# Kernel optimization log

Measured on AMD Instinct MI355X. Metric: run time of the kernel, lower is better.

## Reference

```python
import jax, jax.numpy as jnp
import numpy as np

V, E, Hd, B, S = 50000, 256, 256, 128, 128  # vocab, embed, hidden, batch, seq


def setup_inputs() -> dict:
    key = jax.random.key(0)
    ks = jax.random.split(key, 16)
    std = 1.0 / np.sqrt(Hd)

    def u(k, shape, lim):
        return jax.random.uniform(k, shape, jnp.float32, -lim, lim)

    emb_table = jax.random.normal(ks[0], (V, E), jnp.float32)
    emb_table = emb_table.at[0].set(0.0)  # padding_idx=0

    inp = {
        'batch_size': B,
        'input_Q': jax.random.randint(ks[1], (S, B), 0, V),
        'input_C': jax.random.randint(ks[2], (S, B), 0, V),
        'input_C2': jax.random.randint(ks[3], (S, B), 0, V),
        'hidden_Q': jnp.zeros((2, B, Hd), jnp.float32),
        'cell_Q': jnp.zeros((2, B, Hd), jnp.float32),
        'hidden_C': jnp.zeros((2, B, Hd), jnp.float32),
        'cell_C': jnp.zeros((2, B, Hd), jnp.float32),
        'hidden_C2': jnp.zeros((2, B, Hd), jnp.float32),
        'cell_C2': jnp.zeros((2, B, Hd), jnp.float32),
        'emb_table': emb_table,
        'Wih_f': u(ks[4], (4 * Hd, E), std), 'Whh_f': u(ks[5], (4 * Hd, Hd), std),
        'bih_f': u(ks[6], (4 * Hd,), std), 'bhh_f': u(ks[7], (4 * Hd,), std),
        'Wih_b': u(ks[8], (4 * Hd, E), std), 'Whh_b': u(ks[9], (4 * Hd, Hd), std),
        'bih_b': u(ks[10], (4 * Hd,), std), 'bhh_b': u(ks[11], (4 * Hd,), std),
        'S1_W': u(ks[12], (2 * Hd, 2 * Hd), 0.1),  # init_weights: uniform(-0.1, 0.1)
        'S1_b': u(ks[13], (2 * Hd,), 1.0 / np.sqrt(2 * Hd)),
    }
    return inp


def _lstm_dir(xs, h0, c0, Wih, Whh, b):
    # xs: [S,B,E]; single direction LSTM, torch gate order i,f,g,o
    def step(carry, xt):
        h, c = carry
        g = xt @ Wih.T + h @ Whh.T + b  # [B,4H]
        i, f, gg, o = jnp.split(g, 4, axis=-1)
        c = jax.nn.sigmoid(f) * c + jax.nn.sigmoid(i) * jnp.tanh(gg)
        h = jax.nn.sigmoid(o) * jnp.tanh(c)
        return (h, c), h
    _, ys = jax.lax.scan(step, (h0, c0), xs)
    return ys  # [S,B,H]


def _bilstm(x, h0, c0, Wih_f, Whh_f, bih_f, bhh_f, Wih_b, Whh_b, bih_b, bhh_b):
    # x: [B,S,E] -> [B,S,2H]
    xs = jnp.swapaxes(x, 0, 1)
    yf = _lstm_dir(xs, h0[0], c0[0], Wih_f, Whh_f, bih_f + bhh_f)
    yb = _lstm_dir(xs[::-1], h0[1], c0[1], Wih_b, Whh_b, bih_b + bhh_b)[::-1]
    return jnp.swapaxes(jnp.concatenate([yf, yb], axis=-1), 0, 1)


def _attention(Q, C0, S1_W, S1_b):
    # Batched version of the per-sample loop: Q,C0 [B,S,2H]
    C = jnp.tanh(C0 @ S1_W.T + S1_b)                      # tanh(S1(C0))
    Hm = jnp.einsum('bsd,btd->bst', Q, C)                 # Q @ C.T
    AQ = jax.nn.softmax(Hm, axis=-1)                      # softmax over rows (torch dim=1 for 2D)
    AC = jax.nn.softmax(jnp.swapaxes(Hm, 1, 2), axis=-1)  # softmax(H.T)
    MQ = jnp.einsum('bst,btd->bsd', AQ, Q)
    MC = jnp.einsum('bst,btd->bsd', AC, MQ)
    b = Q.shape[0]
    return MQ.reshape(b, -1), MC.reshape(b, -1)


def reference(batch_size, input_Q, input_C, input_C2, hidden_Q, cell_Q,
              hidden_C, cell_C, hidden_C2, cell_C2, emb_table,
              Wih_f, Whh_f, bih_f, bhh_f, Wih_b, Whh_b, bih_b, bhh_b,
              S1_W, S1_b):
    lstm_w = (Wih_f, Whh_f, bih_f, bhh_f, Wih_b, Whh_b, bih_b, bhh_b)
    # forward() transposes [S,B] -> [B,S] before embedding
    q = emb_table[input_Q.T]
    c = emb_table[input_C.T]
    c2 = emb_table[input_C2.T]
    out_q = _bilstm(q, hidden_Q, cell_Q, *lstm_w)
    out_c = _bilstm(c, hidden_C, cell_C, *lstm_w)
    out_c2 = _bilstm(c2, hidden_C2, cell_C2, *lstm_w)
    attn_Q1, attn_C = _attention(out_q, out_c, S1_W, S1_b)
    attn_Q2, attn_C2 = _attention(out_q, out_c2, S1_W, S1_b)
    return (attn_Q1, attn_C, attn_Q2, attn_C2)
```

## Files before the change

kernel.cpp:

```cpp
#include <hip/hip_runtime.h>
#include <math.h>

namespace {

constexpr int S = 128;
constexpr int B = 128;
constexpr int E = 256;
constexpr int H = 256;

typedef unsigned short u16;
typedef __attribute__((ext_vector_type(8))) short short8v;
typedef __attribute__((ext_vector_type(4))) float f32x4;

__device__ __forceinline__ float sigmoidf(float x) { return 1.0f / (1.0f + expf(-x)); }
__device__ __forceinline__ u16 bf16rnd(float x) {
  unsigned u = __float_as_uint(x);
  return (u16)((u + 0x7FFFu + ((u >> 16) & 1u)) >> 16);
}
__device__ __forceinline__ float bf2f(u16 v) { return __uint_as_float(((unsigned)v) << 16); }
__device__ __forceinline__ void split2(float x, u16& h, u16& l) {
  h = bf16rnd(x);
  l = bf16rnd(x - bf2f(h));
}
__device__ __forceinline__ int gcol_of(int c) {
  return ((c >> 4) & 3) * 256 + ((c & 15) + ((c >> 6) << 4));
}


__global__ void split_pair(const float* __restrict__ src, u16* __restrict__ h,
                           u16* __restrict__ l, long n) {
  long i = (long)blockIdx.x * 256 + threadIdx.x;
  if (i < n) split2(src[i], h[i], l[i]);
}

__global__ void split_w_int(const float* __restrict__ W, u16* __restrict__ h,
                            u16* __restrict__ l) {
  int i = blockIdx.x * 256 + threadIdx.x;
  int c = i >> 8, k = i & 255;
  split2(W[gcol_of(c) * 256 + k], h[i], l[i]);
}

__global__ void make_bint(const float* __restrict__ bih, const float* __restrict__ bhh,
                          float* __restrict__ bint) {
  int c = blockIdx.x * 256 + threadIdx.x;
  int g = gcol_of(c);
  bint[c] = bih[g] + bhh[g];
}

__global__ void init_hc(const float* hQ, const float* cQ, const float* hC, const float* cC,
                        const float* hC2, const float* cC2,
                        u16* hH, u16* hL, float* cst) {
  int i = blockIdx.x * 256 + threadIdx.x;
  if (i >= 6 * B * H) return;
  int z = i / (B * H);
  int rem = i - z * (B * H);
  int input = z >> 1, dir = z & 1;
  const float* hs = input == 0 ? hQ : (input == 1 ? hC : hC2);
  const float* cs = input == 0 ? cQ : (input == 1 ? cC : cC2);
  split2(hs[dir * B * H + rem], hH[i], hL[i]);
  cst[i] = cs[dir * B * H + rem];
}

__global__ void zero_gen(int* gen) {
  if (threadIdx.x < 6) gen[threadIdx.x * 256] = 0;
}


#define MFMA_PROLOG                                        \
  const int tid = threadIdx.x;                             \
  const int wave = tid >> 6, lane = tid & 63;              \
  const int wr = wave >> 1, wc = wave & 1;                 \
  const int lrow = lane & 15, lk = lane >> 4;              \
  f32x4 acc[4][4];

#define MFMA_ZERO_ACC                                      \
  _Pragma("unroll") for (int a_ = 0; a_ < 4; ++a_)         \
  _Pragma("unroll") for (int b_ = 0; b_ < 4; ++b_)         \
      acc[a_][b_] = (f32x4){0.f, 0.f, 0.f, 0.f};

#define MFMA_INNER                                                             \
  __syncthreads();                                                             \
  short8v ah[4], al[4];                                                        \
  _Pragma("unroll") for (int mt = 0; mt < 4; ++mt) {                           \
    int r_ = wr * 64 + mt * 16 + lrow;                                         \
    ah[mt] = *(const short8v*)&Ah[r_ * 40 + lk * 8];                           \
    al[mt] = *(const short8v*)&Al[r_ * 40 + lk * 8];                           \
  }                                                                            \
  _Pragma("unroll") for (int nt = 0; nt < 4; ++nt) {                           \
    int c_ = wc * 64 + nt * 16 + lrow;                                         \
    short8v bh = *(const short8v*)&Bh[c_ * 40 + lk * 8];                       \
    short8v bl = *(const short8v*)&Bl[c_ * 40 + lk * 8];                       \
    _Pragma("unroll") for (int mt = 0; mt < 4; ++mt) {                         \
      acc[mt][nt] = __builtin_amdgcn_mfma_f32_16x16x32_bf16(ah[mt], bh, acc[mt][nt], 0, 0, 0); \
      acc[mt][nt] = __builtin_amdgcn_mfma_f32_16x16x32_bf16(ah[mt], bl, acc[mt][nt], 0, 0, 0); \
      acc[mt][nt] = __builtin_amdgcn_mfma_f32_16x16x32_bf16(al[mt], bh, acc[mt][nt], 0, 0, 0); \
    }                                                                          \
  }

__global__ __launch_bounds__(256) void lstm_fused(
    const int* __restrict__ idxQ, const int* __restrict__ idxC, const int* __restrict__ idxC2,
    const u16* __restrict__ embH, const u16* __restrict__ embL,
    const u16* __restrict__ wihHf, const u16* __restrict__ wihLf,
    const u16* __restrict__ wihHb, const u16* __restrict__ wihLb,
    const u16* __restrict__ whhHf, const u16* __restrict__ whhLf,
    const u16* __restrict__ whhHb, const u16* __restrict__ whhLb,
    const float* __restrict__ bintf, const float* __restrict__ bintb,
    u16* __restrict__ hH, u16* __restrict__ hL, const float* __restrict__ cst0,
    u16* __restrict__ out3h, u16* __restrict__ out3l,
    int* __restrict__ gen)
{
  const int bx = blockIdx.x;
  const int z = bx & 7;
  if (z >= 6) return;
  const int nb = bx >> 3;
  const int input = z >> 1, dir = z & 1;
  const int n0c = nb * 64;
  const int tid = threadIdx.x;
  const int wave = tid >> 6, lane = tid & 63;
  const int lrow = lane & 15, lk = lane >> 4;
  const int wr = wave;
  const int* idx = input == 0 ? idxQ : (input == 1 ? idxC : idxC2);
  const u16* wiHp = dir ? wihHb : wihHf;
  const u16* wiLp = dir ? wihLb : wihLf;
  const u16* whHp = dir ? whhHb : whhHf;
  const u16* whLp = dir ? whhLb : whhLf;
  const float* bint = dir ? bintb : bintf;

  __shared__ __align__(16) short WiH[64 * 264], WiL[64 * 264];
  __shared__ __align__(16) short WhH[64 * 264], WhL[64 * 264];
  __shared__ int tok[128];

#pragma unroll
  for (int i = 0; i < 8; ++i) {
    int e = i * 256 + tid;
    int c = e >> 5, kc = e & 31;
    long src = (long)(n0c + c) * 256 + kc * 8;
    *(short8v*)&WiH[c * 264 + kc * 8] = *(const short8v*)(wiHp + src);
    *(short8v*)&WiL[c * 264 + kc * 8] = *(const short8v*)(wiLp + src);
    *(short8v*)&WhH[c * 264 + kc * 8] = *(const short8v*)(whHp + src);
    *(short8v*)&WhL[c * 264 + kc * 8] = *(const short8v*)(whLp + src);
  }

  const int u = nb * 16 + lrow;
  float bintv[4];
#pragma unroll
  for (int nt = 0; nt < 4; ++nt) bintv[nt] = bint[n0c + nt * 16 + lrow];

  const long HS = (long)6 * B * H;
  const long zb = (long)z * B * H;
  float creg[2][4];
#pragma unroll
  for (int mt = 0; mt < 2; ++mt)
#pragma unroll
    for (int rg = 0; rg < 4; ++rg)
      creg[mt][rg] = cst0[zb + (long)(wr * 32 + mt * 16 + lk * 4 + rg) * H + u];

  int* genz = gen + z * 256;
  u16* o3h = out3h + (long)input * B * S * 512;
  u16* o3l = out3l + (long)input * B * S * 512;

  __syncthreads();

  for (int t = 0; t < S; ++t) {
    const int t_eff = dir ? (S - 1 - t) : t;
    const int par = t & 1;

    if (tid < 128) tok[tid] = idx[t_eff * B + tid];
    __syncthreads();
    const int tv0 = tok[wr * 32 + lrow];
    const int tv1 = tok[wr * 32 + 16 + lrow];

    f32x4 acc[2][4];
#pragma unroll
    for (int mt = 0; mt < 2; ++mt)
#pragma unroll
      for (int nt = 0; nt < 4; ++nt)
        acc[mt][nt] = (f32x4){bintv[nt], bintv[nt], bintv[nt], bintv[nt]};

#pragma unroll
    for (int kb = 0; kb < 8; ++kb) {
      short8v ah[2], al[2];
      {
        long e0 = (long)tv0 * 256 + kb * 32 + lk * 8;
        long e1 = (long)tv1 * 256 + kb * 32 + lk * 8;
        ah[0] = *(const short8v*)(embH + e0);
        al[0] = *(const short8v*)(embL + e0);
        ah[1] = *(const short8v*)(embH + e1);
        al[1] = *(const short8v*)(embL + e1);
      }
#pragma unroll
      for (int nt = 0; nt < 4; ++nt) {
        int c = nt * 16 + lrow;
        short8v bh = *(const short8v*)&WiH[c * 264 + kb * 32 + lk * 8];
        short8v bl = *(const short8v*)&WiL[c * 264 + kb * 32 + lk * 8];
#pragma unroll
        for (int mt = 0; mt < 2; ++mt) {
          acc[mt][nt] = __builtin_amdgcn_mfma_f32_16x16x32_bf16(ah[mt], bh, acc[mt][nt], 0, 0, 0);
          acc[mt][nt] = __builtin_amdgcn_mfma_f32_16x16x32_bf16(ah[mt], bl, acc[mt][nt], 0, 0, 0);
          acc[mt][nt] = __builtin_amdgcn_mfma_f32_16x16x32_bf16(al[mt], bh, acc[mt][nt], 0, 0, 0);
        }
      }
    }

    if (t > 0) {
      if (tid == 0) {
        const int target = 16 * t;
        while (__hip_atomic_load(genz, __ATOMIC_ACQUIRE, __HIP_MEMORY_SCOPE_AGENT) < target) {
          __builtin_amdgcn_s_sleep(2);
        }
      }
      __syncthreads();
    }

    const u16* hrH = hH + (long)par * HS + zb;
    const u16* hrL = hL + (long)par * HS + zb;
#pragma unroll
    for (int kb = 0; kb < 8; ++kb) {
      short8v ah[2], al[2];
#pragma unroll
      for (int mt = 0; mt < 2; ++mt) {
        long ho = (long)(wr * 32 + mt * 16 + lrow) * 256 + kb * 32 + lk * 8;
        ah[mt] = *(const short8v*)(hrH + ho);
        al[mt] = *(const short8v*)(hrL + ho);
      }
#pragma unroll
      for (int nt = 0; nt < 4; ++nt) {
        int c = nt * 16 + lrow;
        short8v bh = *(const short8v*)&WhH[c * 264 + kb * 32 + lk * 8];
        short8v bl = *(const short8v*)&WhL[c * 264 + kb * 32 + lk * 8];
#pragma unroll
        for (int mt = 0; mt < 2; ++mt) {
          acc[mt][nt] = __builtin_amdgcn_mfma_f32_16x16x32_bf16(ah[mt], bh, acc[mt][nt], 0, 0, 0);
          acc[mt][nt] = __builtin_amdgcn_mfma_f32_16x16x32_bf16(ah[mt], bl, acc[mt][nt], 0, 0, 0);
          acc[mt][nt] = __builtin_amdgcn_mfma_f32_16x16x32_bf16(al[mt], bh, acc[mt][nt], 0, 0, 0);
        }
      }
    }

    u16* hwH = hH + (long)(par ^ 1) * HS + zb;
    u16* hwL = hL + (long)(par ^ 1) * HS + zb;
#pragma unroll
    for (int mt = 0; mt < 2; ++mt)
#pragma unroll
      for (int rg = 0; rg < 4; ++rg) {
        int row = wr * 32 + mt * 16 + lk * 4 + rg;
        float ig = sigmoidf(acc[mt][0][rg]);
        float fg = sigmoidf(acc[mt][1][rg]);
        float gg = tanhf(acc[mt][2][rg]);
        float og = sigmoidf(acc[mt][3][rg]);
        float cn = fg * creg[mt][rg] + ig * gg;
        creg[mt][rg] = cn;
        float hn = og * tanhf(cn);
        u16 hh, hl;
        split2(hn, hh, hl);
        long ci = (long)row * H + u;
        hwH[ci] = hh;
        hwL[ci] = hl;
        long oi = ((long)row * S + t_eff) * 512 + dir * 256 + u;
        o3h[oi] = hh;
        o3l[oi] = hl;
      }

    asm volatile("s_waitcnt vmcnt(0)" ::: "memory");
    __syncthreads();
    if (tid == 0) {
      __hip_atomic_fetch_add(genz, 1, __ATOMIC_RELEASE, __HIP_MEMORY_SCOPE_AGENT);
    }
  }
}

__global__ __launch_bounds__(256) void ct_mfma(
    const u16* __restrict__ aH, const u16* __restrict__ aL,
    const u16* __restrict__ s1H, const u16* __restrict__ s1L,
    const float* __restrict__ s1b,
    u16* __restrict__ ctH, u16* __restrict__ ctL)
{
  const int n0 = blockIdx.x * 128, m0 = blockIdx.y * 128;
  __shared__ __align__(16) short Ah[128 * 40], Al[128 * 40], Bh[128 * 40], Bl[128 * 40];
  MFMA_PROLOG
  MFMA_ZERO_ACC

  for (int kb = 0; kb < 512; kb += 32) {
    __syncthreads();
#pragma unroll
    for (int i = 0; i < 2; ++i) {
      int e = i * 256 + tid;
      int r = e >> 2, kg = e & 3;
      long abase = (long)(m0 + r) * 512 + kb + kg * 8;
      *(short8v*)&Ah[r * 40 + kg * 8] = *(const short8v*)(aH + abase);
      *(short8v*)&Al[r * 40 + kg * 8] = *(const short8v*)(aL + abase);
      long bbase = (long)(n0 + r) * 512 + kb + kg * 8;
      *(short8v*)&Bh[r * 40 + kg * 8] = *(const short8v*)(s1H + bbase);
      *(short8v*)&Bl[r * 40 + kg * 8] = *(const short8v*)(s1L + bbase);
    }
    MFMA_INNER
  }

#pragma unroll
  for (int mt = 0; mt < 4; ++mt)
#pragma unroll
    for (int nt = 0; nt < 4; ++nt) {
      int c = n0 + wc * 64 + nt * 16 + lrow;
      float bv = s1b[c];
#pragma unroll
      for (int rg = 0; rg < 4; ++rg) {
        long m = m0 + wr * 64 + mt * 16 + lk * 4 + rg;
        u16 hh, ll;
        split2(tanhf(acc[mt][nt][rg] + bv), hh, ll);
        ctH[m * 512 + c] = hh;
        ctL[m * 512 + c] = ll;
      }
    }
}

__global__ __launch_bounds__(256) void hm_mfma(
    const u16* __restrict__ qH, const u16* __restrict__ qL,
    const u16* __restrict__ ctH, const u16* __restrict__ ctL,
    float* __restrict__ Hm)
{
  const int bb = blockIdx.x;
  const u16* aH = qH + (long)bb * S * 512;
  const u16* aL = qL + (long)bb * S * 512;
  const u16* bH = ctH + (long)bb * S * 512;
  const u16* bL = ctL + (long)bb * S * 512;
  __shared__ __align__(16) short Ah[128 * 40], Al[128 * 40], Bh[128 * 40], Bl[128 * 40];
  MFMA_PROLOG
  MFMA_ZERO_ACC

  for (int kb = 0; kb < 512; kb += 32) {
    __syncthreads();
#pragma unroll
    for (int i = 0; i < 2; ++i) {
      int e = i * 256 + tid;
      int r = e >> 2, kg = e & 3;
      long base = (long)r * 512 + kb + kg * 8;
      *(short8v*)&Ah[r * 40 + kg * 8] = *(const short8v*)(aH + base);
      *(short8v*)&Al[r * 40 + kg * 8] = *(const short8v*)(aL + base);
      *(short8v*)&Bh[r * 40 + kg * 8] = *(const short8v*)(bH + base);
      *(short8v*)&Bl[r * 40 + kg * 8] = *(const short8v*)(bL + base);
    }
    MFMA_INNER
  }

  float* out = Hm + (long)bb * S * S;
#pragma unroll
  for (int mt = 0; mt < 4; ++mt)
#pragma unroll
    for (int nt = 0; nt < 4; ++nt) {
      int c = wc * 64 + nt * 16 + lrow;
#pragma unroll
      for (int rg = 0; rg < 4; ++rg) {
        int m = wr * 64 + mt * 16 + lk * 4 + rg;
        out[(long)m * S + c] = acc[mt][nt][rg];
      }
    }
}

__global__ void transpose_qt(const u16* __restrict__ o3h, const u16* __restrict__ o3l,
                             u16* __restrict__ qth, u16* __restrict__ qtl) {
  const int b = blockIdx.z;
  const int c0 = blockIdx.x * 64, t0 = blockIdx.y * 64;
  __shared__ u16 tile[64][72];
  const int tid = threadIdx.x;
  for (int pl = 0; pl < 2; ++pl) {
    const u16* src = (pl ? o3l : o3h) + (long)b * S * 512;
    u16* dst = (pl ? qtl : qth) + (long)b * 512 * 128;
    __syncthreads();
#pragma unroll
    for (int i = 0; i < 2; ++i) {
      int e = i * 256 + tid;
      int r = e >> 3, sg = e & 7;
      *(short8v*)&tile[r][sg * 8] = *(const short8v*)(src + (long)(t0 + r) * 512 + c0 + sg * 8);
    }
    __syncthreads();
#pragma unroll
    for (int i = 0; i < 2; ++i) {
      int e = i * 256 + tid;
      int c = e >> 3, sg = e & 7;
      short8v v;
#pragma unroll
      for (int j = 0; j < 8; ++j) v[j] = tile[sg * 8 + j][c];
      *(short8v*)(dst + (long)(c0 + c) * 128 + t0 + sg * 8) = v;
    }
  }
}

template <bool WRITE_T>
__global__ __launch_bounds__(256) void pq_mfma(
    const u16* __restrict__ pH, const u16* __restrict__ pL,
    const u16* __restrict__ btH, const u16* __restrict__ btL,
    float* __restrict__ Cout, u16* __restrict__ tH, u16* __restrict__ tL)
{
  const int bb = blockIdx.z, n0 = blockIdx.x * 128;
  const u16* aHp = pH + (long)bb * 128 * 128;
  const u16* aLp = pL + (long)bb * 128 * 128;
  const u16* bHp = btH + ((long)bb * 512 + n0) * 128;
  const u16* bLp = btL + ((long)bb * 512 + n0) * 128;
  __shared__ __align__(16) short Ah[128 * 40], Al[128 * 40], Bh[128 * 40], Bl[128 * 40];
  MFMA_PROLOG
  MFMA_ZERO_ACC

  for (int kb = 0; kb < 128; kb += 32) {
    __syncthreads();
#pragma unroll
    for (int i = 0; i < 2; ++i) {
      int e = i * 256 + tid;
      int r = e >> 2, kg = e & 3;
      long base = (long)r * 128 + kb + kg * 8;
      *(short8v*)&Ah[r * 40 + kg * 8] = *(const short8v*)(aHp + base);
      *(short8v*)&Al[r * 40 + kg * 8] = *(const short8v*)(aLp + base);
      *(short8v*)&Bh[r * 40 + kg * 8] = *(const short8v*)(bHp + base);
      *(short8v*)&Bl[r * 40 + kg * 8] = *(const short8v*)(bLp + base);
    }
    MFMA_INNER
  }

  float* co = Cout + (long)bb * 128 * 512;
#pragma unroll
  for (int mt = 0; mt < 4; ++mt)
#pragma unroll
    for (int nt = 0; nt < 4; ++nt) {
      int c = n0 + wc * 64 + nt * 16 + lrow;
#pragma unroll
      for (int rg = 0; rg < 4; ++rg) {
        int m = wr * 64 + mt * 16 + lk * 4 + rg;
        float v = acc[mt][nt][rg];
        co[(long)m * 512 + c] = v;
        if (WRITE_T) {
          u16 hh, ll;
          split2(v, hh, ll);
          tH[((long)bb * 512 + c) * 128 + m] = hh;
          tL[((long)bb * 512 + c) * 128 + m] = ll;
        }
      }
    }
}

__global__ void softmax_row_bf(const float* __restrict__ Hm, u16* __restrict__ ph,
                               u16* __restrict__ pl) {
  const int row = blockIdx.x;
  const float* p = Hm + (long)row * S;
  const int l = threadIdx.x;
  float v0 = p[l], v1 = p[l + 64];
  float m = fmaxf(v0, v1);
#pragma unroll
  for (int o = 32; o > 0; o >>= 1) m = fmaxf(m, __shfl_xor(m, o));
  float e0 = expf(v0 - m), e1 = expf(v1 - m);
  float s = e0 + e1;
#pragma unroll
  for (int o = 32; o > 0; o >>= 1) s += __shfl_xor(s, o);
  float inv = 1.0f / s;
  u16 hh, ll;
  split2(e0 * inv, hh, ll);
  ph[(long)row * S + l] = hh; pl[(long)row * S + l] = ll;
  split2(e1 * inv, hh, ll);
  ph[(long)row * S + l + 64] = hh; pl[(long)row * S + l + 64] = ll;
}

__global__ void softmax_colT_bf(const float* __restrict__ Hm, u16* __restrict__ ph,
                                u16* __restrict__ pl) {
  const int b = blockIdx.x >> 7;
  const int col = blockIdx.x & 127;
  const float* p = Hm + (long)b * S * S + col;
  const int l = threadIdx.x;
  float v0 = p[(long)l * S], v1 = p[(long)(l + 64) * S];
  float m = fmaxf(v0, v1);
#pragma unroll
  for (int o = 32; o > 0; o >>= 1) m = fmaxf(m, __shfl_xor(m, o));
  float e0 = expf(v0 - m), e1 = expf(v1 - m);
  float s = e0 + e1;
#pragma unroll
  for (int o = 32; o > 0; o >>= 1) s += __shfl_xor(s, o);
  float inv = 1.0f / s;
  long q = ((long)b * S + col) * S;
  u16 hh, ll;
  split2(e0 * inv, hh, ll);
  ph[q + l] = hh; pl[q + l] = ll;
  split2(e1 * inv, hh, ll);
  ph[q + l + 64] = hh; pl[q + l + 64] = ll;
}

__global__ void softmax_row(const float* __restrict__ Hm, float* __restrict__ A) {
  const int row = blockIdx.x;
  const float* p = Hm + (long)row * S;
  const int l = threadIdx.x;
  float v0 = p[l], v1 = p[l + 64];
  float m = fmaxf(v0, v1);
#pragma unroll
  for (int o = 32; o > 0; o >>= 1) m = fmaxf(m, __shfl_xor(m, o));
  float e0 = expf(v0 - m), e1 = expf(v1 - m);
  float s = e0 + e1;
#pragma unroll
  for (int o = 32; o > 0; o >>= 1) s += __shfl_xor(s, o);
  float inv = 1.0f / s;
  float* q = A + (long)row * S;
  q[l] = e0 * inv; q[l + 64] = e1 * inv;
}

__global__ void softmax_colT(const float* __restrict__ Hm, float* __restrict__ A) {
  const int b = blockIdx.x >> 7;
  const int col = blockIdx.x & 127;
  const float* p = Hm + (long)b * S * S + col;
  const int l = threadIdx.x;
  float v0 = p[(long)l * S], v1 = p[(long)(l + 64) * S];
  float m = fmaxf(v0, v1);
#pragma unroll
  for (int o = 32; o > 0; o >>= 1) m = fmaxf(m, __shfl_xor(m, o));
  float e0 = expf(v0 - m), e1 = expf(v1 - m);
  float s = e0 + e1;
#pragma unroll
  for (int o = 32; o > 0; o >>= 1) s += __shfl_xor(s, o);
  float inv = 1.0f / s;
  float* q = A + ((long)b * S + col) * S;
  q[l] = e0 * inv; q[l + 64] = e1 * inv;
}


__global__ void init_state(const float* hQ, const float* cQ,
                           const float* hC, const float* cC,
                           const float* hC2, const float* cC2,
                           float* h0, float* c0) {
  int i = blockIdx.x * 256 + threadIdx.x;
  if (i >= 6 * B * H) return;
  int z = i / (B * H);
  int rem = i - z * (B * H);
  int input = z >> 1, dir = z & 1;
  const float* hs = input == 0 ? hQ : (input == 1 ? hC : hC2);
  const float* cs = input == 0 ? cQ : (input == 1 ? cC : cC2);
  h0[i] = hs[dir * B * H + rem];
  c0[i] = cs[dir * B * H + rem];
}

__global__ __launch_bounds__(256) void lstm_step(
    const int* __restrict__ idxQ, const int* __restrict__ idxC, const int* __restrict__ idxC2,
    const float* __restrict__ emb,
    const float* __restrict__ Wih_f, const float* __restrict__ Whh_f,
    const float* __restrict__ bih_f, const float* __restrict__ bhh_f,
    const float* __restrict__ Wih_b, const float* __restrict__ Whh_b,
    const float* __restrict__ bih_b, const float* __restrict__ bhh_b,
    const float* __restrict__ hread, float* __restrict__ hwrite,
    float* __restrict__ cstate, float* __restrict__ out3, int t)
{
  const int z = blockIdx.z;
  const int input = z >> 1, dir = z & 1;
  const int u0 = blockIdx.x * 16;
  const int b0 = blockIdx.y * 64;
  const int t_eff = dir ? (S - 1 - t) : t;
  const int* idx = input == 0 ? idxQ : (input == 1 ? idxC : idxC2);
  const float* Wih = dir ? Wih_b : Wih_f;
  const float* Whh = dir ? Whh_b : Whh_f;
  const float* bih = dir ? bih_b : bih_f;
  const float* bhh = dir ? bhh_b : bhh_f;

  __shared__ float Alds[64][68];
  __shared__ float Wl[64][68];
  __shared__ int tok[64];

  const int tid = threadIdx.x;
  if (tid < 64) tok[tid] = idx[t_eff * B + b0 + tid];

  const int uu = tid & 15;
  const int rg = tid >> 4;
  const int u = u0 + uu;

  float acc[4][4];
#pragma unroll
  for (int ri = 0; ri < 4; ++ri)
#pragma unroll
    for (int g = 0; g < 4; ++g)
      acc[ri][g] = bih[g * 256 + u] + bhh[g * 256 + u];

  for (int kc = 0; kc < 8; ++kc) {
    __syncthreads();
    if (kc < 4) {
      const int kb = kc * 64;
#pragma unroll
      for (int i = 0; i < 16; ++i) {
        int e = i * 256 + tid;
        int kk = e & 63, r = e >> 6;
        Alds[r][kk] = emb[(long)tok[r] * E + kb + kk];
      }
    } else {
      const int kb = (kc - 4) * 64;
      const float* hs = hread + ((long)z * B + b0) * H + kb;
#pragma unroll
      for (int i = 0; i < 16; ++i) {
        int e = i * 256 + tid;
        int kk = e & 63, r = e >> 6;
        Alds[r][kk] = hs[r * H + kk];
      }
    }
    {
      const float* Wsrc = (kc < 4) ? Wih : Whh;
      const int kb = (kc & 3) * 64;
#pragma unroll
      for (int i = 0; i < 16; ++i) {
        int e = i * 256 + tid;
        int kk = e & 63, c = e >> 6;
        int gcol = (c >> 4) * 256 + u0 + (c & 15);
        Wl[c][kk] = Wsrc[(long)gcol * H + kb + kk];
      }
    }
    __syncthreads();
#pragma unroll
    for (int k4 = 0; k4 < 64; k4 += 4) {
      float4 a[4], w[4];
#pragma unroll
      for (int ri = 0; ri < 4; ++ri) a[ri] = *(const float4*)&Alds[rg * 4 + ri][k4];
#pragma unroll
      for (int g = 0; g < 4; ++g) w[g] = *(const float4*)&Wl[g * 16 + uu][k4];
#pragma unroll
      for (int ri = 0; ri < 4; ++ri)
#pragma unroll
        for (int g = 0; g < 4; ++g)
          acc[ri][g] += a[ri].x * w[g].x + a[ri].y * w[g].y
                      + a[ri].z * w[g].z + a[ri].w * w[g].w;
    }
  }

  float* cs = cstate + (long)z * B * H;
  float* hw = hwrite + (long)z * B * H;
  float* op = out3 + (long)input * B * S * 2 * H;
#pragma unroll
  for (int ri = 0; ri < 4; ++ri) {
    int b = b0 + rg * 4 + ri;
    float ig = sigmoidf(acc[ri][0]);
    float fg = sigmoidf(acc[ri][1]);
    float gg = tanhf(acc[ri][2]);
    float og = sigmoidf(acc[ri][3]);
    float cn = fg * cs[b * H + u] + ig * gg;
    float hn = og * tanhf(cn);
    cs[b * H + u] = cn;
    hw[b * H + u] = hn;
    op[((long)b * S + t_eff) * (2 * H) + dir * H + u] = hn;
  }
}

template <bool TANH>
__global__ __launch_bounds__(256) void gemm_nt(
    const float* __restrict__ A, const float* __restrict__ B_,
    const float* __restrict__ bias, float* __restrict__ C,
    int lda, int ldb, int ldc, int K, long sA, long sB, long sC)
{
  A += blockIdx.z * sA; B_ += blockIdx.z * sB; C += blockIdx.z * sC;
  const int n0 = blockIdx.x * 64, m0 = blockIdx.y * 64;
  __shared__ float Alds[64][68], Blds[64][68];
  const int tid = threadIdx.x, uu = tid & 15, rg = tid >> 4;
  float acc[4][4] = {};
  for (int kb = 0; kb < K; kb += 64) {
    __syncthreads();
#pragma unroll
    for (int i = 0; i < 16; ++i) {
      int e = i * 256 + tid;
      int kk = e & 63, r = e >> 6;
      Alds[r][kk] = A[(long)(m0 + r) * lda + kb + kk];
      Blds[r][kk] = B_[(long)(n0 + r) * ldb + kb + kk];
    }
    __syncthreads();
#pragma unroll
    for (int k4 = 0; k4 < 64; k4 += 4) {
      float4 a[4], w[4];
#pragma unroll
      for (int ri = 0; ri < 4; ++ri) a[ri] = *(const float4*)&Alds[rg * 4 + ri][k4];
#pragma unroll
      for (int ci = 0; ci < 4; ++ci) w[ci] = *(const float4*)&Blds[ci * 16 + uu][k4];
#pragma unroll
      for (int ri = 0; ri < 4; ++ri)
#pragma unroll
        for (int ci = 0; ci < 4; ++ci)
          acc[ri][ci] += a[ri].x * w[ci].x + a[ri].y * w[ci].y
                       + a[ri].z * w[ci].z + a[ri].w * w[ci].w;
    }
  }
#pragma unroll
  for (int ri = 0; ri < 4; ++ri) {
    int m = m0 + rg * 4 + ri;
#pragma unroll
    for (int ci = 0; ci < 4; ++ci) {
      int n = n0 + ci * 16 + uu;
      float v = acc[ri][ci];
      if (bias) v += bias[n];
      if (TANH) v = tanhf(v);
      C[(long)m * ldc + n] = v;
    }
  }
}

__global__ __launch_bounds__(256) void gemm_nn(
    const float* __restrict__ A, const float* __restrict__ B_,
    float* __restrict__ C,
    int lda, int ldb, int ldc, int K, long sA, long sB, long sC)
{
  A += blockIdx.z * sA; B_ += blockIdx.z * sB; C += blockIdx.z * sC;
  const int n0 = blockIdx.x * 64, m0 = blockIdx.y * 64;
  __shared__ float Alds[64][68];
  __shared__ float Blds[64][68];
  const int tid = threadIdx.x, uu = tid & 15, rg = tid >> 4;
  float acc[4][4] = {};
  for (int kb = 0; kb < K; kb += 64) {
    __syncthreads();
#pragma unroll
    for (int i = 0; i < 16; ++i) {
      int e = i * 256 + tid;
      int kk = e & 63, r = e >> 6;
      Alds[r][kk] = A[(long)(m0 + r) * lda + kb + kk];
      Blds[r][kk] = B_[(long)(kb + r) * ldb + n0 + kk];
    }
    __syncthreads();
#pragma unroll
    for (int kk = 0; kk < 64; ++kk) {
      float4 w = *(const float4*)&Blds[kk][uu * 4];
      float a0 = Alds[rg * 4 + 0][kk], a1 = Alds[rg * 4 + 1][kk];
      float a2 = Alds[rg * 4 + 2][kk], a3 = Alds[rg * 4 + 3][kk];
      acc[0][0] += a0 * w.x; acc[0][1] += a0 * w.y; acc[0][2] += a0 * w.z; acc[0][3] += a0 * w.w;
      acc[1][0] += a1 * w.x; acc[1][1] += a1 * w.y; acc[1][2] += a1 * w.z; acc[1][3] += a1 * w.w;
      acc[2][0] += a2 * w.x; acc[2][1] += a2 * w.y; acc[2][2] += a2 * w.z; acc[2][3] += a2 * w.w;
      acc[3][0] += a3 * w.x; acc[3][1] += a3 * w.y; acc[3][2] += a3 * w.z; acc[3][3] += a3 * w.w;
    }
  }
#pragma unroll
  for (int ri = 0; ri < 4; ++ri) {
    int m = m0 + rg * 4 + ri;
    float4 v = make_float4(acc[ri][0], acc[ri][1], acc[ri][2], acc[ri][3]);
    *(float4*)&C[(long)m * ldc + n0 + uu * 4] = v;
  }
}

}

extern "C" void kernel_launch(void* const* d_in, const int* in_sizes, int n_in,
                              void* d_out, int out_size, void* d_ws, size_t ws_size,
                              hipStream_t stream) {
  const int* idxQ    = (const int*)d_in[1];
  const int* idxC    = (const int*)d_in[2];
  const int* idxC2   = (const int*)d_in[3];
  const float* hQ    = (const float*)d_in[4];
  const float* cQ    = (const float*)d_in[5];
  const float* hC    = (const float*)d_in[6];
  const float* cC    = (const float*)d_in[7];
  const float* hC2   = (const float*)d_in[8];
  const float* cC2   = (const float*)d_in[9];
  const float* emb   = (const float*)d_in[10];
  const float* Wih_f = (const float*)d_in[11];
  const float* Whh_f = (const float*)d_in[12];
  const float* bih_f = (const float*)d_in[13];
  const float* bhh_f = (const float*)d_in[14];
  const float* Wih_b = (const float*)d_in[15];
  const float* Whh_b = (const float*)d_in[16];
  const float* bih_b = (const float*)d_in[17];
  const float* bhh_b = (const float*)d_in[18];
  const float* S1W   = (const float*)d_in[19];
  const float* S1b   = (const float*)d_in[20];
  float* out = (float*)d_out;

  const long V = 50000;
  const long OUT1 = (long)B * S * 2 * H;

  size_t off = 0;
  auto alloc = [&](size_t bytes) { size_t o = off; off += (bytes + 255) & ~(size_t)255; return o; };
  const size_t o_o3h  = alloc((size_t)3 * B * S * 512 * 2);
  const size_t o_o3l  = alloc((size_t)3 * B * S * 512 * 2);
  const size_t o_embH = alloc((size_t)V * E * 2);
  const size_t o_embL = alloc((size_t)V * E * 2);
  const size_t o_wihHf = alloc(1024 * 256 * 2), o_wihLf = alloc(1024 * 256 * 2);
  const size_t o_wihHb = alloc(1024 * 256 * 2), o_wihLb = alloc(1024 * 256 * 2);
  const size_t o_whhHf = alloc(1024 * 256 * 2), o_whhLf = alloc(1024 * 256 * 2);
  const size_t o_whhHb = alloc(1024 * 256 * 2), o_whhLb = alloc(1024 * 256 * 2);
  const size_t o_s1H  = alloc(512 * 512 * 2), o_s1L = alloc(512 * 512 * 2);
  const size_t o_bintf = alloc(1024 * 4), o_bintb = alloc(1024 * 4);
  const size_t o_hH   = alloc((size_t)2 * 6 * B * H * 2);
  const size_t o_hL   = alloc((size_t)2 * 6 * B * H * 2);
  const size_t o_cst  = alloc((size_t)6 * B * H * 4);
  const size_t o_gen  = alloc(6 * 256 * 4);
  const size_t o_ctH  = alloc((size_t)B * S * 512 * 2);
  const size_t o_ctL  = alloc((size_t)B * S * 512 * 2);
  const size_t o_Hm   = alloc((size_t)B * S * S * 4);
  const size_t o_Ph   = alloc((size_t)B * S * S * 2);
  const size_t o_Pl   = alloc((size_t)B * S * S * 2);
  const size_t o_QtH  = alloc((size_t)B * 512 * 128 * 2);
  const size_t o_QtL  = alloc((size_t)B * 512 * 128 * 2);
  const size_t o_MQtH = alloc((size_t)B * 512 * 128 * 2);
  const size_t o_MQtL = alloc((size_t)B * 512 * 128 * 2);
  const size_t need_fast = off;

  if (ws_size >= need_fast) {
    char* base = (char*)d_ws;
    u16* o3h = (u16*)(base + o_o3h);
    u16* o3l = (u16*)(base + o_o3l);
    u16* embH = (u16*)(base + o_embH);
    u16* embL = (u16*)(base + o_embL);
    u16* wihHf = (u16*)(base + o_wihHf); u16* wihLf = (u16*)(base + o_wihLf);
    u16* wihHb = (u16*)(base + o_wihHb); u16* wihLb = (u16*)(base + o_wihLb);
    u16* whhHf = (u16*)(base + o_whhHf); u16* whhLf = (u16*)(base + o_whhLf);
    u16* whhHb = (u16*)(base + o_whhHb); u16* whhLb = (u16*)(base + o_whhLb);
    u16* s1H = (u16*)(base + o_s1H); u16* s1L = (u16*)(base + o_s1L);
    float* bintf = (float*)(base + o_bintf);
    float* bintb = (float*)(base + o_bintb);
    u16* hH = (u16*)(base + o_hH);
    u16* hL = (u16*)(base + o_hL);
    float* cst = (float*)(base + o_cst);
    int* gen = (int*)(base + o_gen);
    u16* ctH = (u16*)(base + o_ctH);
    u16* ctL = (u16*)(base + o_ctL);
    float* Hm = (float*)(base + o_Hm);
    u16* Ph = (u16*)(base + o_Ph);
    u16* Pl = (u16*)(base + o_Pl);
    u16* QtH = (u16*)(base + o_QtH);
    u16* QtL = (u16*)(base + o_QtL);
    u16* MQtH = (u16*)(base + o_MQtH);
    u16* MQtL = (u16*)(base + o_MQtL);

    split_pair<<<(int)((V * E + 255) / 256), 256, 0, stream>>>(emb, embH, embL, V * E);
    split_w_int<<<1024, 256, 0, stream>>>(Wih_f, wihHf, wihLf);
    split_w_int<<<1024, 256, 0, stream>>>(Wih_b, wihHb, wihLb);
    split_w_int<<<1024, 256, 0, stream>>>(Whh_f, whhHf, whhLf);
    split_w_int<<<1024, 256, 0, stream>>>(Whh_b, whhHb, whhLb);
    split_pair<<<1024, 256, 0, stream>>>(S1W, s1H, s1L, 512 * 512);
    make_bint<<<4, 256, 0, stream>>>(bih_f, bhh_f, bintf);
    make_bint<<<4, 256, 0, stream>>>(bih_b, bhh_b, bintb);
    init_hc<<<(6 * B * H + 255) / 256, 256, 0, stream>>>(hQ, cQ, hC, cC, hC2, cC2, hH, hL, cst);
    zero_gen<<<1, 64, 0, stream>>>(gen);

    {
      const int* a0 = idxQ; const int* a1 = idxC; const int* a2 = idxC2;
      const u16* a3 = embH; const u16* a4 = embL;
      const u16* a5 = wihHf; const u16* a6 = wihLf;
      const u16* a7 = wihHb; const u16* a8 = wihLb;
      const u16* a9 = whhHf; const u16* a10 = whhLf;
      const u16* a11 = whhHb; const u16* a12 = whhLb;
      const float* a13 = bintf; const float* a14 = bintb;
      u16* a15 = hH; u16* a16 = hL; const float* a17 = cst;
      u16* a18 = o3h; u16* a19 = o3l; int* a20 = gen;
      void* kargs[] = {(void*)&a0, (void*)&a1, (void*)&a2, (void*)&a3, (void*)&a4,
                       (void*)&a5, (void*)&a6, (void*)&a7, (void*)&a8, (void*)&a9,
                       (void*)&a10, (void*)&a11, (void*)&a12, (void*)&a13, (void*)&a14,
                       (void*)&a15, (void*)&a16, (void*)&a17, (void*)&a18, (void*)&a19,
                       (void*)&a20};
      hipLaunchCooperativeKernel((const void*)lstm_fused, dim3(128), dim3(256),
                                 kargs, 0, stream);
    }

    transpose_qt<<<dim3(8, 2, 128), 256, 0, stream>>>(o3h, o3l, QtH, QtL);
    for (int p = 0; p < 2; ++p) {
      const u16* aH = o3h + (size_t)(1 + p) * B * S * 512;
      const u16* aL = o3l + (size_t)(1 + p) * B * S * 512;
      ct_mfma<<<dim3(4, 128), 256, 0, stream>>>(aH, aL, s1H, s1L, S1b, ctH, ctL);
      hm_mfma<<<128, 256, 0, stream>>>(o3h, o3l, ctH, ctL, Hm);
      softmax_row_bf<<<B * S, 64, 0, stream>>>(Hm, Ph, Pl);
      float* MQ = out + (long)(2 * p) * OUT1;
      pq_mfma<true><<<dim3(4, 1, 128), 256, 0, stream>>>(
          Ph, Pl, QtH, QtL, MQ, MQtH, MQtL);
      softmax_colT_bf<<<B * S, 64, 0, stream>>>(Hm, Ph, Pl);
      float* MC = out + (long)(2 * p + 1) * OUT1;
      pq_mfma<false><<<dim3(4, 1, 128), 256, 0, stream>>>(
          Ph, Pl, MQtH, MQtL, MC, nullptr, nullptr);
    }
    return;
  }

  const long ST = (long)6 * B * H;
  float* ws    = (float*)d_ws;
  float* out3  = ws;
  float* hbuf0 = out3 + 3 * OUT1;
  float* hbuf1 = hbuf0 + ST;
  float* cbuf  = hbuf1 + ST;
  float* Ct    = cbuf + ST;
  float* Hm    = Ct + OUT1;
  float* Ab    = Hm + (long)B * S * S;

  init_state<<<(6 * B * H + 255) / 256, 256, 0, stream>>>(hQ, cQ, hC, cC, hC2, cC2, hbuf0, cbuf);

  for (int t = 0; t < S; ++t) {
    float* hr = (t & 1) ? hbuf1 : hbuf0;
    float* hw = (t & 1) ? hbuf0 : hbuf1;
    lstm_step<<<dim3(16, 2, 6), 256, 0, stream>>>(
        idxQ, idxC, idxC2, emb,
        Wih_f, Whh_f, bih_f, bhh_f, Wih_b, Whh_b, bih_b, bhh_b,
        hr, hw, cbuf, out3, t);
  }

  for (int p = 0; p < 2; ++p) {
    const float* Q  = out3;
    const float* C0 = out3 + (long)(1 + p) * OUT1;
    gemm_nt<true><<<dim3(8, 256, 1), 256, 0, stream>>>(
        C0, S1W, S1b, Ct, 512, 512, 512, 512, 0, 0, 0);
    gemm_nt<false><<<dim3(2, 2, B), 256, 0, stream>>>(
        Q, Ct, nullptr, Hm, 512, 512, 128, 512,
        (long)S * 512, (long)S * 512, (long)S * S);
    softmax_row<<<B * S, 64, 0, stream>>>(Hm, Ab);
    float* MQ = out + (long)(2 * p) * OUT1;
    gemm_nn<<<dim3(8, 2, B), 256, 0, stream>>>(
        Ab, Q, MQ, 128, 512, 512, 128,
        (long)S * S, (long)S * 512, (long)S * 512);
    softmax_colT<<<B * S, 64, 0, stream>>>(Hm, Ab);
    float* MC = out + (long)(2 * p + 1) * OUT1;
    gemm_nn<<<dim3(8, 2, B), 256, 0, stream>>>(
        Ab, MQ, MC, 128, 512, 512, 128,
        (long)S * S, (long)S * 512, (long)S * 512);
  }
}
```

Measured before the change: 2.240 ms.

## Pack hidden state hi/lo into 32-bit words with relaxed atomics for cross-block sync

Packs the bf16 hi/lo split of the recurrent hidden state into one 32-bit word so each exchange is a single relaxed atomic store or load instead of two arrays. The spin-wait and generation counter drop from acquire/release to relaxed ordering with a shorter sleep. The per-step token staging through shared memory and its barrier go away, and the output stores move after the generation increment so they no longer delay the signal. Relaxed atomics instead of acquire/release could risk memory-visibility bugs, and the packed loads need extra unpacking ALU work.

```diff
diff --git a/kernel.cpp b/kernel.cpp
--- a/kernel.cpp
+++ b/kernel.cpp
@@ -9,8 +9,10 @@
 constexpr int H = 256;
 
 typedef unsigned short u16;
+typedef unsigned long long u64;
 typedef __attribute__((ext_vector_type(8))) short short8v;
 typedef __attribute__((ext_vector_type(4))) float f32x4;
+typedef __attribute__((ext_vector_type(4))) unsigned uint4v;
 
 __device__ __forceinline__ float sigmoidf(float x) { return 1.0f / (1.0f + expf(-x)); }
 __device__ __forceinline__ u16 bf16rnd(float x) {
@@ -49,7 +51,7 @@
 
 __global__ void init_hc(const float* hQ, const float* cQ, const float* hC, const float* cC,
                         const float* hC2, const float* cC2,
-                        u16* hH, u16* hL, float* cst) {
+                        unsigned* hP, float* cst) {
   int i = blockIdx.x * 256 + threadIdx.x;
   if (i >= 6 * B * H) return;
   int z = i / (B * H);
@@ -57,7 +59,9 @@
   int input = z >> 1, dir = z & 1;
   const float* hs = input == 0 ? hQ : (input == 1 ? hC : hC2);
   const float* cs = input == 0 ? cQ : (input == 1 ? cC : cC2);
-  split2(hs[dir * B * H + rem], hH[i], hL[i]);
+  u16 hh, hl;
+  split2(hs[dir * B * H + rem], hh, hl);
+  hP[i] = ((unsigned)hh << 16) | hl;
   cst[i] = cs[dir * B * H + rem];
 }
 
@@ -105,7 +109,7 @@
     const u16* __restrict__ whhHf, const u16* __restrict__ whhLf,
     const u16* __restrict__ whhHb, const u16* __restrict__ whhLb,
     const float* __restrict__ bintf, const float* __restrict__ bintb,
-    u16* __restrict__ hH, u16* __restrict__ hL, const float* __restrict__ cst0,
+    unsigned* __restrict__ hP, const float* __restrict__ cst0,
     u16* __restrict__ out3h, u16* __restrict__ out3l,
     int* __restrict__ gen)
 {
@@ -128,7 +132,6 @@
 
   __shared__ __align__(16) short WiH[64 * 264], WiL[64 * 264];
   __shared__ __align__(16) short WhH[64 * 264], WhL[64 * 264];
-  __shared__ int tok[128];
 
 #pragma unroll
   for (int i = 0; i < 8; ++i) {
@@ -146,7 +149,7 @@
 #pragma unroll
   for (int nt = 0; nt < 4; ++nt) bintv[nt] = bint[n0c + nt * 16 + lrow];
 
-  const long HS = (long)6 * B * H;
+  const long HS6 = (long)6 * B * H;
   const long zb = (long)z * B * H;
   float creg[2][4];
 #pragma unroll
@@ -165,10 +168,8 @@
     const int t_eff = dir ? (S - 1 - t) : t;
     const int par = t & 1;
 
-    if (tid < 128) tok[tid] = idx[t_eff * B + tid];
-    __syncthreads();
-    const int tv0 = tok[wr * 32 + lrow];
-    const int tv1 = tok[wr * 32 + 16 + lrow];
+    const int tv0 = idx[t_eff * B + wr * 32 + lrow];
+    const int tv1 = idx[t_eff * B + wr * 32 + 16 + lrow];
 
     f32x4 acc[2][4];
 #pragma unroll
@@ -205,23 +206,31 @@
     if (t > 0) {
       if (tid == 0) {
         const int target = 16 * t;
-        while (__hip_atomic_load(genz, __ATOMIC_ACQUIRE, __HIP_MEMORY_SCOPE_AGENT) < target) {
-          __builtin_amdgcn_s_sleep(2);
+        while (__hip_atomic_load(genz, __ATOMIC_RELAXED, __HIP_MEMORY_SCOPE_AGENT) < target) {
+          __builtin_amdgcn_s_sleep(1);
         }
       }
       __syncthreads();
     }
 
-    const u16* hrH = hH + (long)par * HS + zb;
-    const u16* hrL = hL + (long)par * HS + zb;
+    const unsigned* hr = hP + (long)par * HS6 + zb;
 #pragma unroll
     for (int kb = 0; kb < 8; ++kb) {
       short8v ah[2], al[2];
 #pragma unroll
       for (int mt = 0; mt < 2; ++mt) {
-        long ho = (long)(wr * 32 + mt * 16 + lrow) * 256 + kb * 32 + lk * 8;
-        ah[mt] = *(const short8v*)(hrH + ho);
-        al[mt] = *(const short8v*)(hrL + ho);
+        long base = (long)(wr * 32 + mt * 16 + lrow) * 256 + kb * 32 + lk * 8;
+        const u64* p = (const u64*)(hr + base);
+        uint4v hi, lo;
+#pragma unroll
+        for (int j = 0; j < 4; ++j) {
+          u64 q = __hip_atomic_load(p + j, __ATOMIC_RELAXED, __HIP_MEMORY_SCOPE_AGENT);
+          unsigned a = (unsigned)q, b = (unsigned)(q >> 32);
+          hi[j] = (a >> 16) | (b & 0xffff0000u);
+          lo[j] = (a & 0xffffu) | (b << 16);
+        }
+        ah[mt] = __builtin_bit_cast(short8v, hi);
+        al[mt] = __builtin_bit_cast(short8v, lo);
       }
 #pragma unroll
       for (int nt = 0; nt < 4; ++nt) {
@@ -237,8 +246,8 @@
       }
     }
 
-    u16* hwH = hH + (long)(par ^ 1) * HS + zb;
-    u16* hwL = hL + (long)(par ^ 1) * HS + zb;
+    unsigned* hw = hP + (long)(par ^ 1) * HS6 + zb;
+    u16 oh[2][4], ol[2][4];
 #pragma unroll
     for (int mt = 0; mt < 2; ++mt)
 #pragma unroll
@@ -253,19 +262,26 @@
         float hn = og * tanhf(cn);
         u16 hh, hl;
         split2(hn, hh, hl);
-        long ci = (long)row * H + u;
-        hwH[ci] = hh;
-        hwL[ci] = hl;
+        oh[mt][rg] = hh; ol[mt][rg] = hl;
+        __hip_atomic_store(&hw[(long)row * H + u], ((unsigned)hh << 16) | hl,
+                           __ATOMIC_RELAXED, __HIP_MEMORY_SCOPE_AGENT);
+      }
+
+    asm volatile("s_waitcnt vmcnt(0)" ::: "memory");
+    __syncthreads();
+    if (tid == 0) {
+      __hip_atomic_fetch_add(genz, 1, __ATOMIC_RELAXED, __HIP_MEMORY_SCOPE_AGENT);
+    }
+
+#pragma unroll
+    for (int mt = 0; mt < 2; ++mt)
+#pragma unroll
+      for (int rg = 0; rg < 4; ++rg) {
+        int row = wr * 32 + mt * 16 + lk * 4 + rg;
         long oi = ((long)row * S + t_eff) * 512 + dir * 256 + u;
-        o3h[oi] = hh;
-        o3l[oi] = hl;
-      }
-
-    asm volatile("s_waitcnt vmcnt(0)" ::: "memory");
-    __syncthreads();
-    if (tid == 0) {
-      __hip_atomic_fetch_add(genz, 1, __ATOMIC_RELEASE, __HIP_MEMORY_SCOPE_AGENT);
-    }
+        o3h[oi] = oh[mt][rg];
+        o3l[oi] = ol[mt][rg];
+      }
   }
 }
 
@@ -768,8 +784,7 @@
   const size_t o_whhHb = alloc(1024 * 256 * 2), o_whhLb = alloc(1024 * 256 * 2);
   const size_t o_s1H  = alloc(512 * 512 * 2), o_s1L = alloc(512 * 512 * 2);
   const size_t o_bintf = alloc(1024 * 4), o_bintb = alloc(1024 * 4);
-  const size_t o_hH   = alloc((size_t)2 * 6 * B * H * 2);
-  const size_t o_hL   = alloc((size_t)2 * 6 * B * H * 2);
+  const size_t o_hP   = alloc((size_t)2 * 6 * B * H * 4);
   const size_t o_cst  = alloc((size_t)6 * B * H * 4);
   const size_t o_gen  = alloc(6 * 256 * 4);
   const size_t o_ctH  = alloc((size_t)B * S * 512 * 2);
@@ -796,8 +811,7 @@
     u16* s1H = (u16*)(base + o_s1H); u16* s1L = (u16*)(base + o_s1L);
     float* bintf = (float*)(base + o_bintf);
     float* bintb = (float*)(base + o_bintb);
-    u16* hH = (u16*)(base + o_hH);
-    u16* hL = (u16*)(base + o_hL);
+    unsigned* hP = (unsigned*)(base + o_hP);
     float* cst = (float*)(base + o_cst);
     int* gen = (int*)(base + o_gen);
     u16* ctH = (u16*)(base + o_ctH);
@@ -818,7 +832,7 @@
     split_pair<<<1024, 256, 0, stream>>>(S1W, s1H, s1L, 512 * 512);
     make_bint<<<4, 256, 0, stream>>>(bih_f, bhh_f, bintf);
     make_bint<<<4, 256, 0, stream>>>(bih_b, bhh_b, bintb);
-    init_hc<<<(6 * B * H + 255) / 256, 256, 0, stream>>>(hQ, cQ, hC, cC, hC2, cC2, hH, hL, cst);
+    init_hc<<<(6 * B * H + 255) / 256, 256, 0, stream>>>(hQ, cQ, hC, cC, hC2, cC2, hP, cst);
     zero_gen<<<1, 64, 0, stream>>>(gen);
 
     {
@@ -829,13 +843,12 @@
       const u16* a9 = whhHf; const u16* a10 = whhLf;
       const u16* a11 = whhHb; const u16* a12 = whhLb;
       const float* a13 = bintf; const float* a14 = bintb;
-      u16* a15 = hH; u16* a16 = hL; const float* a17 = cst;
-      u16* a18 = o3h; u16* a19 = o3l; int* a20 = gen;
+      unsigned* a15 = hP; const float* a16 = cst;
+      u16* a17 = o3h; u16* a18 = o3l; int* a19 = gen;
       void* kargs[] = {(void*)&a0, (void*)&a1, (void*)&a2, (void*)&a3, (void*)&a4,
                        (void*)&a5, (void*)&a6, (void*)&a7, (void*)&a8, (void*)&a9,
                        (void*)&a10, (void*)&a11, (void*)&a12, (void*)&a13, (void*)&a14,
-                       (void*)&a15, (void*)&a16, (void*)&a17, (void*)&a18, (void*)&a19,
-                       (void*)&a20};
+                       (void*)&a15, (void*)&a16, (void*)&a17, (void*)&a18, (void*)&a19};
       hipLaunchCooperativeKernel((const void*)lstm_fused, dim3(128), dim3(256),
                                  kargs, 0, stream);
     }
```

Result: slower. 2.478 ms (+10.6%).
